# Kernel tuning notes

Hardware: AMD Instinct MI355X
Metric: run time of the kernel (lower is better)

Reference implementation:

```python
import jax, jax.numpy as jnp
import numpy as np

APERTURE = 128
LN_EPS = 1e-6

def _layer_norm(y, g, b):
    mu = jnp.mean(y, axis=-1, keepdims=True)
    var = jnp.var(y, axis=-1, keepdims=True)
    return (y - mu) / jnp.sqrt(var + LN_EPS) * g + b

def setup_inputs() -> dict:
    key = jax.random.key(0)
    ks = jax.random.split(key, 12)
    B, S, D = 4, 4096, 1024
    gain = np.sqrt(2.0)
    xav = lambda k, fan_out, fan_in: jax.random.uniform(
        k, (fan_out, fan_in), jnp.float32,
        -gain * np.sqrt(6.0 / (fan_in + fan_out)), gain * np.sqrt(6.0 / (fan_in + fan_out)))
    return {
        "x": jax.random.normal(ks[0], (B, S, D), jnp.float32),
        "Wq": xav(ks[1], D, D),
        "Wk": xav(ks[2], D, D),
        "Wv": xav(ks[3], D, D),
        "Wo": xav(ks[4], D, D),
        "k1_w": xav(ks[5], D, D),
        "k1_b": jnp.full((D,), 0.1, jnp.float32),
        "k2_w": xav(ks[6], 1, D),
        "k2_b": jnp.full((1,), 0.1, jnp.float32),
        "ln_g": jnp.ones((D,), jnp.float32),
        "ln_b": jnp.zeros((D,), jnp.float32),
    }

def reference(x, Wq, Wk, Wv, Wo, k1_w, k1_b, k2_w, k2_b, ln_g, ln_b):
    B, S, D = x.shape
    scale = jnp.float32(1.0 / np.sqrt(D))
    neg_inf = jnp.float32(-np.inf)

    Q = x @ Wq.T  # [B,S,D]
    K = x @ Wk.T
    V = x @ Wv.T

    e = jnp.einsum('bsd,btd->bst', Q, K) * scale  # [B,S,S]

    # ignore_self: -inf on the diagonal
    i = jnp.arange(S)[:, None]
    j = jnp.arange(S)[None, :]
    e = jnp.where(i == j, neg_inf, e)

    # banded aperture mask: tril(e, ap) * triu(e, -ap); zeros of the product -> -inf
    d = j - i
    scope = jnp.where(d <= APERTURE, e, 0.0) * jnp.where(d >= -APERTURE, e, 0.0)
    e = jnp.where(scope == 0.0, neg_inf, e)

    alpha = jax.nn.softmax(e, axis=2)
    c = jnp.einsum('bst,btd->bsd', alpha, V)
    c = c @ Wo.T

    y = c + x
    y = _layer_norm(y, ln_g, ln_b)
    y = jax.nn.relu(y @ k1_w.T + k1_b)
    y = _layer_norm(y, ln_g, ln_b)
    y = jax.nn.sigmoid(y @ k2_w.T + k2_b)  # [B,S,1]
    return y.reshape(B, S)
```

## Files before the change

kernel.cpp:

```cpp
#include <hip/hip_runtime.h>
#include <math.h>

#define DD 1024
#define SS 4096
#define AP 128
#define LN_EPS 1e-6f
#define BK 32
#define BAND 384

typedef __bf16 bf16;
typedef __attribute__((ext_vector_type(4))) __bf16 bf16x4;
typedef __attribute__((ext_vector_type(8))) __bf16 bf16x8;
typedef __attribute__((ext_vector_type(4))) float f32x4;

#define GLOAD_LDS16(g, l)                                                   \
    __builtin_amdgcn_global_load_lds(                                        \
        (const __attribute__((address_space(1))) void*)(g),                  \
        (__attribute__((address_space(3))) void*)(l), 16, 0, 0)

__global__ __launch_bounds__(256) void prep_all(const float* __restrict__ x,
                                                const float* __restrict__ Wq,
                                                const float* __restrict__ Wk,
                                                const float* __restrict__ Wv,
                                                const float* __restrict__ Wo,
                                                const float* __restrict__ k1w,
                                                const float* __restrict__ k1b,
                                                const float* __restrict__ lng,
                                                const float* __restrict__ lnb,
                                                bf16* __restrict__ xb,
                                                bf16* __restrict__ Wob,
                                                bf16* __restrict__ k1g,
                                                bf16* __restrict__ Wtb,
                                                float* __restrict__ u1,
                                                float* __restrict__ c1b) {
    __shared__ float tile[64][65];
    const int bid = blockIdx.x;
    const int tid = threadIdx.x;
    if (bid < 16384) {
        const int i = (bid * 256 + tid) * 4;
        const float4 a = *(const float4*)(x + i);
        bf16x4 o;
        o[0] = (__bf16)a.x; o[1] = (__bf16)a.y; o[2] = (__bf16)a.z; o[3] = (__bf16)a.w;
        *(bf16x4*)(xb + i) = o;
        return;
    }
    if (bid < 18432) {
        const int b2 = bid - 16384;
        const int sel = b2 >> 10;
        const int bb = b2 & 1023;
        const float* s = sel ? k1w : Wo;
        bf16* d = sel ? k1g : Wob;
        const int i = (bb * 256 + tid) * 4;
        float4 a = *(const float4*)(s + i);
        if (sel) {
            const float4 g4 = *(const float4*)(lng + (i & (DD - 1)));
            a.x *= g4.x; a.y *= g4.y; a.z *= g4.z; a.w *= g4.w;
        }
        bf16x4 o;
        o[0] = (__bf16)a.x; o[1] = (__bf16)a.y; o[2] = (__bf16)a.z; o[3] = (__bf16)a.w;
        *(bf16x4*)(d + i) = o;
        return;
    }
    if (bid < 19200) {
        const int t = bid - 18432;
        const int tz = t >> 8;
        const int tb_ = t & 255;
        const float* in = (tz == 0) ? Wq : (tz == 1) ? Wk : Wv;
        bf16* out = Wtb + ((size_t)tz << 20);
        const int r0 = (tb_ >> 4) * 64, c0 = (tb_ & 15) * 64;
        const int lr = tid >> 4;
        const int lc = (tid & 15) * 4;
#pragma unroll
        for (int rr = 0; rr < 4; rr++) {
            const int row = lr + rr * 16;
            const float4 v = *(const float4*)(in + (size_t)(r0 + row) * DD + c0 + lc);
            tile[row][lc] = v.x; tile[row][lc + 1] = v.y;
            tile[row][lc + 2] = v.z; tile[row][lc + 3] = v.w;
        }
        __syncthreads();
#pragma unroll
        for (int rr = 0; rr < 4; rr++) {
            const int row = lr + rr * 16;
            bf16x4 o;
            o[0] = (__bf16)tile[lc + 0][row];
            o[1] = (__bf16)tile[lc + 1][row];
            o[2] = (__bf16)tile[lc + 2][row];
            o[3] = (__bf16)tile[lc + 3][row];
            *(bf16x4*)(out + (size_t)(c0 + row) * DD + r0 + lc) = o;
        }
        return;
    }
    const int pv = bid - 19200;
    const int lane = tid & 63, wave = tid >> 6;
    const int n = pv * 4 + wave;
    const float* row = k1w + (size_t)n * DD + lane * 16;
    float su = 0.f, sb = 0.f;
#pragma unroll
    for (int q = 0; q < 4; q++) {
        const float4 a = *(const float4*)(row + q * 4);
        const float4 g4 = *(const float4*)(lng + lane * 16 + q * 4);
        const float4 b4 = *(const float4*)(lnb + lane * 16 + q * 4);
        su += a.x * g4.x + a.y * g4.y + a.z * g4.z + a.w * g4.w;
        sb += a.x * b4.x + a.y * b4.y + a.z * b4.z + a.w * b4.w;
    }
#pragma unroll
    for (int off = 32; off > 0; off >>= 1) {
        su += __shfl_xor(su, off);
        sb += __shfl_xor(sb, off);
    }
    if (lane == 0) {
        u1[n] = su;
        c1b[n] = sb + k1b[n];
    }
}

__global__ __launch_bounds__(256) void gemm_pair(const bf16* __restrict__ A0,
                                                 const bf16* __restrict__ W0,
                                                 bf16* __restrict__ O0,
                                                 const bf16* __restrict__ A1,
                                                 const bf16* __restrict__ W1,
                                                 bf16* __restrict__ O1) {
    const bf16* A = blockIdx.z ? A1 : A0;
    const bf16* W = blockIdx.z ? W1 : W0;
    bf16* O = blockIdx.z ? O1 : O0;
    __shared__ bf16 As[128 * BK];
    __shared__ bf16 Bs[128 * BK];
    const int tid = threadIdx.x;
    const int lane = tid & 63;
    const int wave = tid >> 6;
    const int wm = wave & 1;
    const int wn = wave >> 1;
    const int m0 = blockIdx.y * 128;
    const int n0 = blockIdx.x * 128;

    const int c = wave * 64 + lane;
    const int ar = c >> 2;
    const int ac = (c & 3) << 3;
    char* AsB = (char*)As;
    char* BsB = (char*)Bs;
    const int lr = lane & 15;
    const int lk = (lane >> 4) << 3;

    f32x4 acc[4][4] = {};

    for (int kt = 0; kt < DD; kt += BK) {
        const bf16* ga0 = A + (size_t)(m0 + ar) * DD + kt + ac;
        const bf16* gb0 = W + (size_t)(n0 + ar) * DD + kt + ac;
        GLOAD_LDS16(ga0, AsB + wave * 1024);
        GLOAD_LDS16(ga0 + (size_t)64 * DD, AsB + 4096 + wave * 1024);
        GLOAD_LDS16(gb0, BsB + wave * 1024);
        GLOAD_LDS16(gb0 + (size_t)64 * DD, BsB + 4096 + wave * 1024);
        __syncthreads();

        bf16x8 af[4], bfr[4];
#pragma unroll
        for (int i = 0; i < 4; i++)
            af[i] = *(const bf16x8*)&As[(wm * 64 + i * 16 + lr) * BK + lk];
#pragma unroll
        for (int j = 0; j < 4; j++)
            bfr[j] = *(const bf16x8*)&Bs[(wn * 64 + j * 16 + lr) * BK + lk];
#pragma unroll
        for (int i = 0; i < 4; i++)
#pragma unroll
            for (int j = 0; j < 4; j++)
                acc[i][j] = __builtin_amdgcn_mfma_f32_16x16x32_bf16(af[i], bfr[j], acc[i][j], 0, 0, 0);
        __syncthreads();
    }

#pragma unroll
    for (int i = 0; i < 4; i++) {
        const int row = m0 + wm * 64 + i * 16 + ((lane >> 4) << 2);
#pragma unroll
        for (int j = 0; j < 4; j++) {
            const int col = n0 + wn * 64 + j * 16 + (lane & 15);
#pragma unroll
            for (int rr = 0; rr < 4; rr++)
                O[(size_t)(row + rr) * DD + col] = (__bf16)acc[i][j][rr];
        }
    }
}


#define KL_STAGE_A(tt, hh, bb)                                               \
    {                                                                        \
        const bf16* gp_ = Aop + gofsA + (tt) * 64 + (hh) * 32;               \
        GLOAD_LDS16(gp_, smem + (bb) + (hh) * 16384 + ldsW);                 \
        GLOAD_LDS16(gp_ + (size_t)128 * DD,                                  \
                    smem + (bb) + (hh) * 16384 + 8192 + ldsW);               \
    }
#define KL_STAGE_B(tt, hh, bb)                                               \
    {                                                                        \
        const bf16* gp_ = Bop + gofsB + (tt) * 64 + (hh) * 32;               \
        GLOAD_LDS16(gp_, smem + (bb) + 32768 + (hh) * 16384 + ldsW);         \
        GLOAD_LDS16(gp_ + (size_t)128 * DD,                                  \
                    smem + (bb) + 32768 + (hh) * 16384 + 8192 + ldsW);       \
    }
#define KL_READS(AR, BR, OFF)                                                \
    _Pragma("unroll") for (int q_ = 0; q_ < 8; q_++)                         \
        AR[q_] = *(const bf16x8*)(sA + (OFF) + (q_ >> 2) * 4096 + (q_ & 3) * 1024); \
    _Pragma("unroll") for (int j_ = 0; j_ < 4; j_++)                         \
        BR[j_] = *(const bf16x8*)(sB + (OFF) + j_ * 1024);
#define KL_MFMA32(AR, BR)                                                    \
    __builtin_amdgcn_s_setprio(1);                                           \
    _Pragma("unroll") for (int q_ = 0; q_ < 8; q_++)                         \
        _Pragma("unroll") for (int j_ = 0; j_ < 4; j_++)                     \
            acc[q_][j_] = __builtin_amdgcn_mfma_f32_16x16x32_bf16(AR[q_], BR[j_], acc[q_][j_], 0, 0, 0); \
    __builtin_amdgcn_s_setprio(0);
#define KL_BARRIER(N) asm volatile("s_waitcnt vmcnt(" #N ")\n\ts_barrier" ::: "memory")
#define KL_FENCE __builtin_amdgcn_sched_barrier(0)

__device__ __forceinline__ void kloop256(const bf16* __restrict__ Aop,
                                         const bf16* __restrict__ Bop,
                                         const int m0, const int n0,
                                         char* smem, f32x4 (&acc)[8][4],
                                         const int tid, const int lane,
                                         const int wave, const int wm, const int wn) {
    const int grow = tid >> 2;
    const int gslot = (tid & 3) ^ ((tid >> 3) & 3);
    const size_t gofsA = (size_t)(m0 + grow) * DD + gslot * 8;
    const size_t gofsB = (size_t)(n0 + grow) * DD + gslot * 8;
    const int ldsW = wave * 1024;
    const int sxo = (((lane >> 4) ^ ((lane >> 1) & 3)) << 4);
    const char* sA = smem + wm * 8192 + (lane & 15) * 64 + sxo;
    const char* sB = smem + 32768 + wn * 4096 + (lane & 15) * 64 + sxo;

    bf16x8 A0[8], B0[4], A1[8], B1[4];

    KL_STAGE_A(0, 0, 0) KL_STAGE_B(0, 0, 0)
    KL_STAGE_A(0, 1, 0) KL_STAGE_B(0, 1, 0)
    KL_STAGE_A(1, 0, 65536) KL_STAGE_B(1, 0, 65536)
    KL_BARRIER(4);
    KL_READS(A0, B0, 0)

    int bufo = 0;
    for (int t = 0; t < 14; t++) {
        const int nb = bufo ^ 65536;
        KL_READS(A1, B1, bufo + 16384)
        KL_STAGE_A(t + 1, 1, nb) KL_STAGE_B(t + 1, 1, nb)
        KL_FENCE;
        KL_MFMA32(A0, B0)
        KL_BARRIER(4);
        KL_READS(A0, B0, nb)
        KL_STAGE_A(t + 2, 0, bufo) KL_STAGE_B(t + 2, 0, bufo)
        KL_FENCE;
        KL_MFMA32(A1, B1)
        KL_BARRIER(4);
        bufo = nb;
    }
    {
        const int nb = bufo ^ 65536;
        KL_READS(A1, B1, bufo + 16384)
        KL_STAGE_A(15, 1, nb) KL_STAGE_B(15, 1, nb)
        KL_FENCE;
        KL_MFMA32(A0, B0)
        KL_BARRIER(4);
        KL_READS(A0, B0, nb)
        KL_FENCE;
        KL_MFMA32(A1, B1)
        KL_BARRIER(0);
        KL_READS(A1, B1, nb + 16384)
        KL_FENCE;
        KL_MFMA32(A0, B0)
        KL_MFMA32(A1, B1)
    }
}

__global__ __launch_bounds__(512) void gemm_uv(const bf16* __restrict__ xb,
                                               const bf16* __restrict__ Gt,
                                               const bf16* __restrict__ W2,
                                               bf16* __restrict__ Ub,
                                               bf16* __restrict__ Vt2) {
    __shared__ char smem[131072];
    int id = blockIdx.x;
    const bf16* A;
    const bf16* W;
    bf16* O;
    int m0, n0;
    size_t ldo;
    if (id < 256) {
        A = xb; W = Gt; O = Ub;
        m0 = (id & 63) * 256; n0 = (id >> 6) * 256; ldo = DD;
    } else {
        id -= 256;
        A = W2; W = xb; O = Vt2;
        m0 = (id >> 6) * 256; n0 = (id & 63) * 256; ldo = (size_t)4 * SS;
    }
    const int tid = threadIdx.x;
    const int lane = tid & 63;
    const int wave = tid >> 6;
    const int wm = wave & 1;
    const int wn = wave >> 1;

    f32x4 acc[8][4] = {};
    kloop256(A, W, m0, n0, smem, acc, tid, lane, wave, wm, wn);

#pragma unroll
    for (int a = 0; a < 8; a++) {
        const int row = m0 + wm * 128 + a * 16 + ((lane >> 4) << 2);
#pragma unroll
        for (int j = 0; j < 4; j++) {
            const int col = n0 + wn * 64 + j * 16 + (lane & 15);
#pragma unroll
            for (int rr = 0; rr < 4; rr++)
                O[(size_t)(row + rr) * ldo + col] = (__bf16)acc[a][j][rr];
        }
    }
}

__global__ __launch_bounds__(512) void gemm_k1(const bf16* __restrict__ T,
                                               const bf16* __restrict__ k1g,
                                               const float* __restrict__ part_t,
                                               const float* __restrict__ u1,
                                               const float* __restrict__ c1b,
                                               const float* __restrict__ lng,
                                               const float* __restrict__ k2w,
                                               float* __restrict__ part_h) {
    __shared__ char smem[131072];
    __shared__ float lmu[256], lrs[256];
    const int m0 = blockIdx.x * 256;
    const int n0 = blockIdx.y * 256;
    const int tid = threadIdx.x;
    const int lane = tid & 63;
    const int wave = tid >> 6;
    const int wm = wave & 1;
    const int wn = wave >> 1;

    if (tid < 256) {
        const float* p = part_t + (size_t)(m0 + tid) * 32;
        float s1 = 0.f, s2 = 0.f;
#pragma unroll
        for (int s = 0; s < 8; s++) {
            const float4 v = *(const float4*)(p + s * 4);
            s1 += v.x + v.z;
            s2 += v.y + v.w;
        }
        const float m = s1 * (1.f / DD);
        lmu[tid] = m;
        lrs[tid] = rsqrtf(s2 * (1.f / DD) - m * m + LN_EPS);
    }
    __syncthreads();

    f32x4 acc[8][4] = {};
    kloop256(T, k1g, m0, n0, smem, acc, tid, lane, wave, wm, wn);

    float u1v[4], cbv[4], ugv[4];
#pragma unroll
    for (int j = 0; j < 4; j++) {
        const int col = n0 + wn * 64 + j * 16 + (lane & 15);
        u1v[j] = u1[col];
        cbv[j] = c1b[col];
        ugv[j] = lng[col] * k2w[col];
    }
    const int strip = blockIdx.y * 4 + wn;
#pragma unroll
    for (int a = 0; a < 8; a++) {
#pragma unroll
        for (int rr = 0; rr < 4; rr++) {
            const int lrow = wm * 128 + a * 16 + ((lane >> 4) << 2) + rr;
            const int row = m0 + lrow;
            const float mr = lmu[lrow], rs = lrs[lrow];
            float s1 = 0.f, s2 = 0.f, s3 = 0.f;
#pragma unroll
            for (int j = 0; j < 4; j++) {
                const float v = rs * (acc[a][j][rr] - mr * u1v[j]) + cbv[j];
                const float h = fmaxf(v, 0.f);
                s1 += h; s2 += h * h; s3 += h * ugv[j];
            }
#pragma unroll
            for (int off = 8; off > 0; off >>= 1) {
                s1 += __shfl_xor(s1, off);
                s2 += __shfl_xor(s2, off);
                s3 += __shfl_xor(s3, off);
            }
            if ((lane & 15) == 0) {
                float* p = part_h + (size_t)row * 48 + strip * 3;
                p[0] = s1; p[1] = s2; p[2] = s3;
            }
        }
    }
}

__global__ __launch_bounds__(256) void attn_s_mfma(const bf16* __restrict__ U,
                                                   const bf16* __restrict__ X,
                                                   float* __restrict__ S) {
    __shared__ bf16 As[128 * BK];
    __shared__ bf16 Bs[128 * BK];
    const int tid = threadIdx.x;
    const int lane = tid & 63;
    const int wave = tid >> 6;
    const int wm = wave & 1;
    const int wn = wave >> 1;
    const int t = blockIdx.x;
    const int nb = blockIdx.y;
    const int m0 = t * 128;
    const long w0 = (long)t * 128 - 128 + (long)nb * 128;

    const int c = wave * 64 + lane;
    const int ar = c >> 2;
    const int ac = (c & 3) << 3;
    char* AsB = (char*)As;
    char* BsB = (char*)Bs;
    const int lr = lane & 15;
    const int lk = (lane >> 4) << 3;

    f32x4 acc[4][4] = {};

    for (int kt = 0; kt < DD; kt += BK) {
        const bf16* ga0 = U + (size_t)(m0 + ar) * DD + kt + ac;
        const bf16* gb0 = X + (w0 + ar) * DD + kt + ac;
        GLOAD_LDS16(ga0, AsB + wave * 1024);
        GLOAD_LDS16(ga0 + (size_t)64 * DD, AsB + 4096 + wave * 1024);
        GLOAD_LDS16(gb0, BsB + wave * 1024);
        GLOAD_LDS16(gb0 + (size_t)64 * DD, BsB + 4096 + wave * 1024);
        __syncthreads();

        bf16x8 af[4], bfr[4];
#pragma unroll
        for (int i = 0; i < 4; i++)
            af[i] = *(const bf16x8*)&As[(wm * 64 + i * 16 + lr) * BK + lk];
#pragma unroll
        for (int j = 0; j < 4; j++)
            bfr[j] = *(const bf16x8*)&Bs[(wn * 64 + j * 16 + lr) * BK + lk];
#pragma unroll
        for (int i = 0; i < 4; i++)
#pragma unroll
            for (int j = 0; j < 4; j++)
                acc[i][j] = __builtin_amdgcn_mfma_f32_16x16x32_bf16(af[i], bfr[j], acc[i][j], 0, 0, 0);
        __syncthreads();
    }

#pragma unroll
    for (int i = 0; i < 4; i++) {
        const int row = m0 + wm * 64 + i * 16 + ((lane >> 4) << 2);
#pragma unroll
        for (int j = 0; j < 4; j++) {
            const int col = nb * 128 + wn * 64 + j * 16 + (lane & 15);
#pragma unroll
            for (int rr = 0; rr < 4; rr++)
                S[(size_t)(row + rr) * BAND + col] = acc[i][j][rr];
        }
    }
}

__global__ __launch_bounds__(256) void attn_softmax(const float* __restrict__ S,
                                                    bf16* __restrict__ P) {
    const int wave = threadIdx.x >> 6;
    const int lane = threadIdx.x & 63;
    const int g = blockIdx.x * 4 + wave;
    const int i = g & (SS - 1);
    const int j_start = ((i >> 7) << 7) - 128;
    const float scale = 0.03125f;
    float s[6];
    float m = -INFINITY;
#pragma unroll
    for (int t = 0; t < 6; t++) {
        const int jj = lane + t * 64;
        const int j = j_start + jj;
        const int dj = j - i;
        const bool valid = (j >= 0) && (j < SS) && (dj != 0) && (dj <= AP) && (dj >= -AP);
        const float v = S[(size_t)g * BAND + jj] * scale;
        s[t] = valid ? v : -INFINITY;
        m = fmaxf(m, s[t]);
    }
#pragma unroll
    for (int off = 32; off > 0; off >>= 1) m = fmaxf(m, __shfl_xor(m, off));
    float l = 0.f;
#pragma unroll
    for (int t = 0; t < 6; t++) {
        s[t] = __expf(s[t] - m);
        l += s[t];
    }
#pragma unroll
    for (int off = 32; off > 0; off >>= 1) l += __shfl_xor(l, off);
    const float inv = 1.f / l;
#pragma unroll
    for (int t = 0; t < 6; t++)
        P[(size_t)g * BAND + lane + t * 64] = (__bf16)(s[t] * inv);
}

__global__ __launch_bounds__(512) void attn_pv_mfma(const bf16* __restrict__ P,
                                                    const bf16* __restrict__ Vt,
                                                    const bf16* __restrict__ xres,
                                                    bf16* __restrict__ T,
                                                    float* __restrict__ part_t) {
    __shared__ bf16 As[128 * BK];
    __shared__ bf16 Bs[256 * BK];
    const int tid = threadIdx.x;
    const int lane = tid & 63;
    const int wave = tid >> 6;
    const int wm = wave & 1;
    const int wn = wave >> 1;
    const int t = blockIdx.x;
    const int m0 = t * 128;
    const int n0 = blockIdx.y * 256;
    const bf16* Wb = Vt + (long)t * 128 - 128;

    const int ar = tid >> 2;
    const int ac = (tid & 3) << 3;
    char* AsB = (char*)As;
    char* BsB = (char*)Bs;
    const int lr = lane & 15;
    const int lk = (lane >> 4) << 3;

    f32x4 acc[4][4] = {};

    for (int kt = 0; kt < BAND; kt += BK) {
        const bf16* ga0 = P + (size_t)(m0 + ar) * BAND + kt + ac;
        const bf16* gb0 = Wb + (size_t)(n0 + ar) * (4 * SS) + kt + ac;
        GLOAD_LDS16(ga0, AsB + wave * 1024);
        GLOAD_LDS16(gb0, BsB + wave * 1024);
        GLOAD_LDS16(gb0 + (size_t)128 * (4 * SS), BsB + 8192 + wave * 1024);
        __syncthreads();

        bf16x8 af[4], bfr[4];
#pragma unroll
        for (int i = 0; i < 4; i++)
            af[i] = *(const bf16x8*)&As[(wm * 64 + i * 16 + lr) * BK + lk];
#pragma unroll
        for (int j = 0; j < 4; j++)
            bfr[j] = *(const bf16x8*)&Bs[(wn * 64 + j * 16 + lr) * BK + lk];
#pragma unroll
        for (int i = 0; i < 4; i++)
#pragma unroll
            for (int j = 0; j < 4; j++)
                acc[i][j] = __builtin_amdgcn_mfma_f32_16x16x32_bf16(af[i], bfr[j], acc[i][j], 0, 0, 0);
        __syncthreads();
    }

    const int strip = blockIdx.y * 4 + wn;
#pragma unroll
    for (int i = 0; i < 4; i++) {
#pragma unroll
        for (int rr = 0; rr < 4; rr++) {
            const int row = m0 + wm * 64 + i * 16 + ((lane >> 4) << 2) + rr;
            float s1 = 0.f, s2 = 0.f;
#pragma unroll
            for (int j = 0; j < 4; j++) {
                const int col = n0 + wn * 64 + j * 16 + (lane & 15);
                const size_t idx = (size_t)row * DD + col;
                const __bf16 tv_b = (__bf16)(acc[i][j][rr] + (float)xres[idx]);
                T[idx] = tv_b;
                const float tv = (float)tv_b;
                s1 += tv; s2 += tv * tv;
            }
#pragma unroll
            for (int off = 8; off > 0; off >>= 1) {
                s1 += __shfl_xor(s1, off);
                s2 += __shfl_xor(s2, off);
            }
            if ((lane & 15) == 0) {
                float2 st; st.x = s1; st.y = s2;
                *(float2*)(part_t + (size_t)row * 32 + strip * 2) = st;
            }
        }
    }
}

__global__ __launch_bounds__(256) void ln_k2_p(const float* __restrict__ part_h,
                                               const float* __restrict__ g,
                                               const float* __restrict__ bta,
                                               const float* __restrict__ w2,
                                               const float* __restrict__ b2,
                                               float* __restrict__ out) {
    __shared__ float red[256], red2[256];
    const int tid = threadIdx.x;
    const float4 g4 = *(const float4*)(g + tid * 4);
    const float4 w4 = *(const float4*)(w2 + tid * 4);
    const float4 b4 = *(const float4*)(bta + tid * 4);
    red[tid] = g4.x * w4.x + g4.y * w4.y + g4.z * w4.z + g4.w * w4.w;
    red2[tid] = b4.x * w4.x + b4.y * w4.y + b4.z * w4.z + b4.w * w4.w;
    __syncthreads();
    for (int s = 128; s > 0; s >>= 1) {
        if (tid < s) { red[tid] += red[tid + s]; red2[tid] += red2[tid + s]; }
        __syncthreads();
    }
    const float sum_u = red[0];
    const float sum_bw = red2[0];

    const int r = blockIdx.x * 256 + tid;
    const float* p = part_h + (size_t)r * 48;
    float s1 = 0.f, s2 = 0.f, s3 = 0.f;
#pragma unroll
    for (int s = 0; s < 16; s++) {
        s1 += p[s * 3 + 0];
        s2 += p[s * 3 + 1];
        s3 += p[s * 3 + 2];
    }
    const float m = s1 * (1.f / DD);
    const float var = s2 * (1.f / DD) - m * m;
    const float rs = rsqrtf(var + LN_EPS);
    const float z = rs * (s3 - m * sum_u) + sum_bw + b2[0];
    out[r] = 1.f / (1.f + __expf(-z));
}

extern "C" void kernel_launch(void* const* d_in, const int* in_sizes, int n_in,
                              void* d_out, int out_size, void* d_ws, size_t ws_size,
                              hipStream_t stream) {
    const float* x   = (const float*)d_in[0];
    const float* Wq  = (const float*)d_in[1];
    const float* Wk  = (const float*)d_in[2];
    const float* Wv  = (const float*)d_in[3];
    const float* Wo  = (const float*)d_in[4];
    const float* k1w = (const float*)d_in[5];
    const float* k1b = (const float*)d_in[6];
    const float* k2w = (const float*)d_in[7];
    const float* k2b = (const float*)d_in[8];
    const float* lng = (const float*)d_in[9];
    const float* lnb = (const float*)d_in[10];
    float* out = (float*)d_out;

    const int N = 4 * SS;
    char* ws = (char*)d_ws;
    bf16*  Ub   = (bf16*)(ws);
    bf16*  xb   = (bf16*)(ws + ((size_t)32  << 20));
    bf16*  Vt2  = (bf16*)(ws + ((size_t)64  << 20));
    bf16*  P    = (bf16*)(ws + ((size_t)96  << 20));
    float* S    = (float*)(ws + ((size_t)108 << 20));
    bf16*  T    = (bf16*)(ws + ((size_t)164 << 20));
    bf16*  Wtb  = (bf16*)(ws + ((size_t)196 << 20));
    bf16*  Wqtb = Wtb;
    bf16*  Wktb = Wqtb + (1 << 20);
    bf16*  Wvtb = Wktb + (1 << 20);
    bf16*  Wob  = Wvtb + (1 << 20);
    bf16*  k1g  = Wob  + (1 << 20);
    bf16*  Gtb  = k1g  + (1 << 20);
    bf16*  W2b  = Gtb  + (1 << 20);
    float* u1     = (float*)(ws + ((size_t)210 << 20));
    float* c1b    = u1 + DD;
    float* part_t = (float*)(ws + ((size_t)211 << 20));
    float* part_h = (float*)(ws + ((size_t)214 << 20));

    dim3 tb(256);

    prep_all<<<19456, tb, 0, stream>>>(x, Wq, Wk, Wv, Wo, k1w, k1b, lng, lnb,
                                       xb, Wob, k1g, Wtb, u1, c1b);

    gemm_pair<<<dim3(8, 8, 2), tb, 0, stream>>>(Wktb, Wqtb, Gtb, Wob, Wvtb, W2b);

    gemm_uv<<<512, dim3(512), 0, stream>>>(xb, Gtb, W2b, Ub, Vt2);

    attn_s_mfma<<<dim3(N / 128, 3), tb, 0, stream>>>(Ub, xb, S);
    attn_softmax<<<N / 4, tb, 0, stream>>>(S, P);
    attn_pv_mfma<<<dim3(N / 128, 4), dim3(512), 0, stream>>>(P, Vt2, xb, T, part_t);

    gemm_k1<<<dim3(64, 4), dim3(512), 0, stream>>>(T, k1g, part_t, u1, c1b, lng, k2w, part_h);
    ln_k2_p<<<N / 256, tb, 0, stream>>>(part_h, lng, lnb, k2w, k2b, out);
}
```

Baseline: 324.0 us.

## Restructure GEMM k-loop into eight-phase ping-pong schedule with smaller fragments

Rewrites the 256x256 bf16 GEMM main loop. The old loop held two full sets of A/B register fragments; the new one loads four A and four B fragments at a time and splits each k-step into quarter phases of 16 MFMAs. Each phase pairs one global-to-LDS stage with s_barrier plus lgkmcnt waits, which lowers register pressure and interleaves loads more finely. The cost is many more barriers per iteration and the loss of register double-buffering between LDS reads and MFMAs, which may expose LDS latency.

```diff
diff --git a/kernel.cpp b/kernel.cpp
--- a/kernel.cpp
+++ b/kernel.cpp
@@ -195,19 +195,35 @@
         GLOAD_LDS16(gp_ + (size_t)128 * DD,                                  \
                     smem + (bb) + 32768 + (hh) * 16384 + 8192 + ldsW);       \
     }
-#define KL_READS(AR, BR, OFF)                                                \
-    _Pragma("unroll") for (int q_ = 0; q_ < 8; q_++)                         \
-        AR[q_] = *(const bf16x8*)(sA + (OFF) + (q_ >> 2) * 4096 + (q_ & 3) * 1024); \
-    _Pragma("unroll") for (int j_ = 0; j_ < 4; j_++)                         \
-        BR[j_] = *(const bf16x8*)(sB + (OFF) + j_ * 1024);
-#define KL_MFMA32(AR, BR)                                                    \
+#define KL_RD_A4(ah, OFF)                                                    \
+    af[0] = *(const bf16x8*)(sA + (OFF) + (ah) * 4096 + 0);                  \
+    af[1] = *(const bf16x8*)(sA + (OFF) + (ah) * 4096 + 1024);               \
+    af[2] = *(const bf16x8*)(sA + (OFF) + (ah) * 4096 + 2048);               \
+    af[3] = *(const bf16x8*)(sA + (OFF) + (ah) * 4096 + 3072);
+#define KL_RD_B4(OFF)                                                        \
+    bfr[0] = *(const bf16x8*)(sB + (OFF) + 0);                               \
+    bfr[1] = *(const bf16x8*)(sB + (OFF) + 1024);                            \
+    bfr[2] = *(const bf16x8*)(sB + (OFF) + 2048);                            \
+    bfr[3] = *(const bf16x8*)(sB + (OFF) + 3072);
+#define KL_MM16(ah)                                                          \
     __builtin_amdgcn_s_setprio(1);                                           \
-    _Pragma("unroll") for (int q_ = 0; q_ < 8; q_++)                         \
+    _Pragma("unroll") for (int i_ = 0; i_ < 4; i_++)                         \
         _Pragma("unroll") for (int j_ = 0; j_ < 4; j_++)                     \
-            acc[q_][j_] = __builtin_amdgcn_mfma_f32_16x16x32_bf16(AR[q_], BR[j_], acc[q_][j_], 0, 0, 0); \
-    __builtin_amdgcn_s_setprio(0);
-#define KL_BARRIER(N) asm volatile("s_waitcnt vmcnt(" #N ")\n\ts_barrier" ::: "memory")
-#define KL_FENCE __builtin_amdgcn_sched_barrier(0)
+            acc[(ah) * 4 + i_][j_] = __builtin_amdgcn_mfma_f32_16x16x32_bf16(\
+                af[i_], bfr[j_], acc[(ah) * 4 + i_][j_], 0, 0, 0);           \
+    __builtin_amdgcn_s_setprio(0);                                           \
+    __builtin_amdgcn_sched_barrier(0);
+#define KL_VM(N) asm volatile("s_waitcnt vmcnt(" #N ")" ::: "memory")
+#define KL_BAR                                                               \
+    do {                                                                     \
+        __builtin_amdgcn_sched_barrier(0);                                   \
+        __builtin_amdgcn_s_barrier();                                        \
+    } while (0)
+#define KL_LG0                                                               \
+    do {                                                                     \
+        asm volatile("s_waitcnt lgkmcnt(0)" ::: "memory");                   \
+        __builtin_amdgcn_sched_barrier(0);                                   \
+    } while (0)
 
 __device__ __forceinline__ void kloop256(const bf16* __restrict__ Aop,
                                          const bf16* __restrict__ Bop,
@@ -224,44 +240,80 @@
     const char* sA = smem + wm * 8192 + (lane & 15) * 64 + sxo;
     const char* sB = smem + 32768 + wn * 4096 + (lane & 15) * 64 + sxo;
 
-    bf16x8 A0[8], B0[4], A1[8], B1[4];
-
-    KL_STAGE_A(0, 0, 0) KL_STAGE_B(0, 0, 0)
-    KL_STAGE_A(0, 1, 0) KL_STAGE_B(0, 1, 0)
-    KL_STAGE_A(1, 0, 65536) KL_STAGE_B(1, 0, 65536)
-    KL_BARRIER(4);
-    KL_READS(A0, B0, 0)
-
-    int bufo = 0;
+    bf16x8 af[4], bfr[4];
+
+    KL_STAGE_B(0, 0, 0) KL_STAGE_A(0, 0, 0)
+    KL_STAGE_B(0, 1, 0) KL_STAGE_A(0, 1, 0)
+    KL_STAGE_B(1, 0, 65536) KL_STAGE_A(1, 0, 65536)
+    KL_STAGE_B(1, 1, 65536)
+    KL_VM(6);
+    KL_BAR;
+
+#pragma unroll 1
     for (int t = 0; t < 14; t++) {
+        const int bufo = (t & 1) * 65536;
         const int nb = bufo ^ 65536;
-        KL_READS(A1, B1, bufo + 16384)
-        KL_STAGE_A(t + 1, 1, nb) KL_STAGE_B(t + 1, 1, nb)
-        KL_FENCE;
-        KL_MFMA32(A0, B0)
-        KL_BARRIER(4);
-        KL_READS(A0, B0, nb)
-        KL_STAGE_A(t + 2, 0, bufo) KL_STAGE_B(t + 2, 0, bufo)
-        KL_FENCE;
-        KL_MFMA32(A1, B1)
-        KL_BARRIER(4);
-        bufo = nb;
+        KL_VM(6);
+        KL_RD_A4(0, bufo) KL_RD_B4(bufo)
+        KL_STAGE_A(t + 1, 1, nb)
+        KL_BAR; KL_LG0;
+        KL_MM16(0)
+        KL_BAR;
+        KL_RD_A4(1, bufo)
+        KL_STAGE_B(t + 2, 0, bufo)
+        KL_BAR; KL_LG0;
+        KL_MM16(1)
+        KL_BAR;
+        KL_VM(6);
+        KL_RD_A4(0, bufo + 16384) KL_RD_B4(bufo + 16384)
+        KL_STAGE_A(t + 2, 0, bufo)
+        KL_BAR; KL_LG0;
+        KL_MM16(0)
+        KL_BAR;
+        KL_RD_A4(1, bufo + 16384)
+        KL_STAGE_B(t + 2, 1, bufo)
+        KL_BAR; KL_LG0;
+        KL_MM16(1)
+        KL_BAR;
     }
     {
-        const int nb = bufo ^ 65536;
-        KL_READS(A1, B1, bufo + 16384)
-        KL_STAGE_A(15, 1, nb) KL_STAGE_B(15, 1, nb)
-        KL_FENCE;
-        KL_MFMA32(A0, B0)
-        KL_BARRIER(4);
-        KL_READS(A0, B0, nb)
-        KL_FENCE;
-        KL_MFMA32(A1, B1)
-        KL_BARRIER(0);
-        KL_READS(A1, B1, nb + 16384)
-        KL_FENCE;
-        KL_MFMA32(A0, B0)
-        KL_MFMA32(A1, B1)
+        KL_VM(6);
+        KL_RD_A4(0, 0) KL_RD_B4(0)
+        KL_STAGE_A(15, 1, 65536)
+        KL_BAR; KL_LG0;
+        KL_MM16(0)
+        KL_BAR;
+        KL_RD_A4(1, 0)
+        KL_BAR; KL_LG0;
+        KL_MM16(1)
+        KL_BAR;
+        KL_VM(4);
+        KL_RD_A4(0, 16384) KL_RD_B4(16384)
+        KL_BAR; KL_LG0;
+        KL_MM16(0)
+        KL_BAR;
+        KL_RD_A4(1, 16384)
+        KL_BAR; KL_LG0;
+        KL_MM16(1)
+        KL_BAR;
+    }
+    {
+        KL_VM(0);
+        KL_RD_A4(0, 65536) KL_RD_B4(65536)
+        KL_BAR; KL_LG0;
+        KL_MM16(0)
+        KL_BAR;
+        KL_RD_A4(1, 65536)
+        KL_BAR; KL_LG0;
+        KL_MM16(1)
+        KL_BAR;
+        KL_RD_A4(0, 65536 + 16384) KL_RD_B4(65536 + 16384)
+        KL_BAR; KL_LG0;
+        KL_MM16(0)
+        KL_BAR;
+        KL_RD_A4(1, 65536 + 16384)
+        KL_BAR; KL_LG0;
+        KL_MM16(1)
     }
 }
 
```

Result: slower. 344.0 us (+6.2%).
